# Kernel optimization log

Hardware: AMD Instinct MI355X
Metric: run time of the kernel (lower is better)

The kernel has to match this reference:

```python
import jax, jax.numpy as jnp
import numpy as np

# Module hyperparameters (init_kwargs)
NUM_EXPERTS = 8
HIDDEN = 1024
CAP_FACTORS = [0.5, 0.75, 1.0, 1.0, 1.25, 1.25, 1.5, 1.5]


def setup_inputs() -> dict:
    key = jax.random.key(0)
    k1, k2, k3 = jax.random.split(key, 3)
    G, T = 4, 2048
    token_inputs = jax.random.normal(k1, (G, T, HIDDEN), dtype=jnp.float32)
    # RouterWeights = nn.Linear(hidden, num_experts, bias=True)
    W = jax.random.normal(k2, (HIDDEN, NUM_EXPERTS), dtype=jnp.float32) * (1.0 / np.sqrt(HIDDEN))
    b = jax.random.normal(k3, (NUM_EXPERTS,), dtype=jnp.float32) * 0.01
    return {"token_inputs": token_inputs, "W": W, "b": b, "expert_capacity": 256}


def reference(token_inputs, W, b, expert_capacity):
    # token_inputs: [G, T, H]; jitter_noise=0 so no jitter; ignore_padding_tokens=False
    G, T, _ = token_inputs.shape
    logits = jnp.einsum("gth,he->gte", token_inputs, W) + b  # [G, T, E]
    probs = jax.nn.softmax(logits, axis=-1)
    # router z-loss: mean(logsumexp(logits, -1)^2)
    z_loss = jnp.mean(jax.nn.logsumexp(logits, axis=-1) ** 2)

    capacities = [int(expert_capacity * f) for f in CAP_FACTORS]
    max_cap = max(capacities)

    dispatch_slices = []  # each [G, T, max_cap] int32
    combine_slices = []   # each [G, T, max_cap] float32
    for e, cap in enumerate(capacities):
        gate, idx = jax.lax.top_k(probs[:, :, e], cap)  # [G, cap]
        # one_hot(idx, T): [G, cap, T] -> transpose to [G, T, cap]
        oh = jax.nn.one_hot(idx, T, dtype=jnp.int32).transpose(0, 2, 1)  # [G, T, cap]
        oh = jnp.pad(oh, ((0, 0), (0, 0), (0, max_cap - cap)))
        dispatch_slices.append(oh)
        # combine: gate broadcast over tokens dim (as in original code)
        comb = jnp.broadcast_to(gate[:, None, :], (G, T, cap))  # [G, T, cap]
        comb = jnp.pad(comb, ((0, 0), (0, 0), (0, max_cap - cap)))
        combine_slices.append(comb)

    dispatch_mask = jnp.stack(dispatch_slices, axis=1)  # [G, E, T, max_cap]
    combine_array = jnp.stack(combine_slices, axis=1).astype(jnp.float32)  # [G, E, T, max_cap]
    auxiliary_loss = jnp.float32(0.0)
    return dispatch_mask, combine_array, auxiliary_loss, z_loss
```

## Files before the change

kernel.cpp:

```cpp
#include <hip/hip_runtime.h>
#include <hip/hip_bf16.h>
#include <math.h>

#define G 4
#define T 2048
#define H 1024
#define E 8
#define NBUK 2048
#define SELB 32
#define K1B 512
#define K2B 256
#define K3B 256
#define SCB 12

typedef float f4 __attribute__((ext_vector_type(4)));
typedef unsigned long long u64;


__global__ __launch_bounds__(256) void k1_logits(
    const float* __restrict__ x, const float* __restrict__ W,
    const float* __restrict__ b, u64* __restrict__ keys,
    float* __restrict__ lse2) {
  int slot = (int)(blockIdx.x * 4 + (threadIdx.x >> 6));
  int lane = (int)(threadIdx.x & 63);

  for (int wave = slot; wave < G * T; wave += K1B * 4) {
    const float* xr = x + (size_t)wave * H;
    double acc0 = 0, acc1 = 0, acc2 = 0, acc3 = 0;
    double acc4 = 0, acc5 = 0, acc6 = 0, acc7 = 0;
#pragma unroll
    for (int j = 0; j < 4; ++j) {
      int hbase = j * 256 + lane * 4;
      f4 xv = *(const f4*)(xr + hbase);
#pragma unroll
      for (int k = 0; k < 4; ++k) {
        const float* wr = W + (size_t)(hbase + k) * 8;
        f4 w0 = *(const f4*)(wr);
        f4 w1 = *(const f4*)(wr + 4);
        double xd = (double)xv[k];
        acc0 += xd * (double)w0[0];
        acc1 += xd * (double)w0[1];
        acc2 += xd * (double)w0[2];
        acc3 += xd * (double)w0[3];
        acc4 += xd * (double)w1[0];
        acc5 += xd * (double)w1[1];
        acc6 += xd * (double)w1[2];
        acc7 += xd * (double)w1[3];
      }
    }
#pragma unroll
    for (int off = 32; off >= 1; off >>= 1) {
      acc0 += __shfl_xor(acc0, off);
      acc1 += __shfl_xor(acc1, off);
      acc2 += __shfl_xor(acc2, off);
      acc3 += __shfl_xor(acc3, off);
      acc4 += __shfl_xor(acc4, off);
      acc5 += __shfl_xor(acc5, off);
      acc6 += __shfl_xor(acc6, off);
      acc7 += __shfl_xor(acc7, off);
    }
    double l0 = acc0 + (double)b[0], l1 = acc1 + (double)b[1];
    double l2 = acc2 + (double)b[2], l3 = acc3 + (double)b[3];
    double l4 = acc4 + (double)b[4], l5 = acc5 + (double)b[5];
    double l6 = acc6 + (double)b[6], l7 = acc7 + (double)b[7];
    double m = fmax(fmax(fmax(l0, l1), fmax(l2, l3)),
                    fmax(fmax(l4, l5), fmax(l6, l7)));
    double la = (lane & 1) ? l1 : l0;
    double lb = (lane & 1) ? l3 : l2;
    double lc = (lane & 1) ? l5 : l4;
    double ld = (lane & 1) ? l7 : l6;
    double le = (lane & 2) ? lb : la;
    double lf = (lane & 2) ? ld : lc;
    double lsel = (lane & 4) ? lf : le;

    double pe = exp(lsel - m);
    double s = pe;
    s += __shfl_xor(s, 1);
    s += __shfl_xor(s, 2);
    s += __shfl_xor(s, 4);
    double inv = 1.0 / s;
    float pf = (float)(pe * inv);

    int g = wave >> 11;
    int t = wave & (T - 1);
    if (lane < 8) {
      keys[((size_t)g * 8 + lane) * T + t] =
          ((u64)__float_as_uint(pf) << 32) | (unsigned)(~t);
    }
    if (lane == 0) {
      double lse = m + log(s);
      lse2[wave] = (float)(lse * lse);
    }
  }
}

__global__ __launch_bounds__(1024) void k2_select_zero(
    const u64* __restrict__ keys, float* __restrict__ gate,
    int* __restrict__ idx, float* __restrict__ out, unsigned n4d, int max_cap,
    int ec) {
  unsigned bid = blockIdx.x;
  unsigned tid = threadIdx.x;

  if (bid >= SELB) {
    f4* outD = (f4*)out;
    f4 z = {0.0f, 0.0f, 0.0f, 0.0f};
    unsigned stride = (K2B - SELB) * 1024u;
    for (unsigned i = (bid - SELB) * 1024u + tid; i < n4d; i += stride)
      outD[i] = z;
    return;
  }

  __shared__ int hist[NBUK];
  __shared__ int sA[NBUK];
  __shared__ int sB[NBUK];
  __shared__ int cur[NBUK];
  __shared__ u64 srt[T];
  int ge = (int)bid;

  hist[tid] = 0;
  hist[tid + 1024] = 0;
  if (tid < (unsigned)max_cap) {
    gate[(size_t)ge * max_cap + tid] = 0.0f;
    idx[(size_t)ge * max_cap + tid] = -1;
  }
  __syncthreads();

  const u64* kcol = keys + (size_t)ge * T;
  u64 k0 = kcol[tid];
  u64 k1 = kcol[tid + 1024];
  int b0 = (int)(k0 >> 53);
  int b1 = (int)(k1 >> 53);
  atomicAdd(&hist[b0], 1);
  atomicAdd(&hist[b1], 1);
  __syncthreads();

  sA[tid] = hist[tid];
  sA[tid + 1024] = hist[tid + 1024];
  __syncthreads();
  int* src = sA;
  int* dst = sB;
  for (int s = 1; s < NBUK; s <<= 1) {
    for (int i = (int)tid; i < NBUK; i += 1024) {
      int v = src[i];
      if (i + s < NBUK) v += src[i + s];
      dst[i] = v;
    }
    __syncthreads();
    int* tmp = src;
    src = dst;
    dst = tmp;
  }
  for (int i = (int)tid; i < NBUK; i += 1024) cur[i] = src[i] - hist[i];
  __syncthreads();

  int p0 = atomicAdd(&cur[b0], 1);
  srt[p0] = k0;
  int p1 = atomicAdd(&cur[b1], 1);
  srt[p1] = k1;
  __syncthreads();

  const double factors[8] = {0.5, 0.75, 1.0, 1.0, 1.25, 1.25, 1.5, 1.5};
  int cap = (int)((double)ec * factors[ge & 7]);

  int o0 = src[b0] - hist[b0];
  if (o0 < cap) {
    int end = src[b0];
    int c = 0;
    for (int i = o0; i < end; ++i) c += (int)(srt[i] > k0);
    int r = o0 + c;
    if (r < cap) {
      gate[(size_t)ge * max_cap + r] = __uint_as_float((unsigned)(k0 >> 32));
      idx[(size_t)ge * max_cap + r] = (int)~(unsigned)k0;
    }
  }
  int o1 = src[b1] - hist[b1];
  if (o1 < cap) {
    int end = src[b1];
    int c = 0;
    for (int i = o1; i < end; ++i) c += (int)(srt[i] > k1);
    int r = o1 + c;
    if (r < cap) {
      gate[(size_t)ge * max_cap + r] = __uint_as_float((unsigned)(k1 >> 32));
      idx[(size_t)ge * max_cap + r] = (int)~(unsigned)k1;
    }
  }
}

template <int MC4S>
__global__ __launch_bounds__(1024) void k3_scatter_combine(
    const float* __restrict__ gate, const int* __restrict__ idx,
    const float* __restrict__ lse2, float* __restrict__ out, unsigned n4d,
    unsigned mc4_rt, int max_cap) {
  const unsigned mc4 = MC4S ? (unsigned)MC4S : mc4_rt;
  unsigned tid = threadIdx.x;
  unsigned bid = blockIdx.x;

  if (bid == 0) {
    __shared__ double red[256];
    if (tid < 256) {
      double s = 0.0;
      for (int i = tid; i < G * T; i += 256) s += (double)lse2[i];
      red[tid] = s;
    }
    __syncthreads();
    for (int off = 128; off > 0; off >>= 1) {
      if ((int)tid < off) red[tid] += red[tid + off];
      __syncthreads();
    }
    if (tid == 0) {
      size_t ne = (size_t)n4d * 4;
      out[2 * ne] = 0.0f;
      out[2 * ne + 1] = (float)(red[0] / (double)(G * T));
    }
    return;
  }
  if (bid <= SCB) {
    unsigned s = (bid - 1) * 1024u + tid;
    if (s < (unsigned)(G * E) * (unsigned)max_cap) {
      unsigned ge = s / (unsigned)max_cap;
      unsigned c = s - ge * (unsigned)max_cap;
      int t = idx[s];
      if (t >= 0) out[((size_t)ge * T + t) * (unsigned)max_cap + c] = 1.0f;
    }
    return;
  }

  f4* outC = (f4*)out + n4d;
  const f4* gate4 = (const f4*)gate;
  unsigned fb = bid - 1 - SCB;
  unsigned nfb = K3B - 1 - SCB;
  unsigned stride = nfb * 1024u;
  for (unsigned i = fb * 1024u + tid; i < n4d; i += stride) {
    unsigned c4 = i % mc4;
    unsigned ge = (i / mc4) >> 11;
    outC[i] = gate4[ge * mc4 + c4];
  }
}

extern "C" void kernel_launch(void* const* d_in, const int* in_sizes, int n_in,
                              void* d_out, int out_size, void* d_ws,
                              size_t ws_size, hipStream_t stream) {
  const float* x = (const float*)d_in[0];
  const float* W = (const float*)d_in[1];
  const float* b = (const float*)d_in[2];

  long long body = (long long)out_size - 2;
  int max_cap = (int)(body / (2LL * G * E * T));
  if (max_cap <= 0) return;
  int ec = (2 * max_cap) / 3;

  u64* keys = (u64*)d_ws;
  float* lse2 = (float*)(keys + (size_t)G * E * T);
  float* gate = lse2 + (size_t)G * T;
  int* idx = (int*)(gate + (size_t)G * E * max_cap);

  unsigned n4d = (unsigned)((long long)G * E * T * max_cap / 4);

  k1_logits<<<K1B, 256, 0, stream>>>(x, W, b, keys, lse2);
  k2_select_zero<<<K2B, 1024, 0, stream>>>(keys, gate, idx, (float*)d_out,
                                           n4d, max_cap, ec);
  if (max_cap == 384) {
    k3_scatter_combine<96><<<K3B, 1024, 0, stream>>>(gate, idx, lse2,
                                                     (float*)d_out, n4d, 96u,
                                                     max_cap);
  } else {
    k3_scatter_combine<0><<<K3B, 1024, 0, stream>>>(
        gate, idx, lse2, (float*)d_out, n4d, (unsigned)(max_cap / 4), max_cap);
  }
}
```

Measured before the change: 80.59 us.

## Fuse three router kernels into one persistent kernel with grid barriers

Merges the logits/softmax, top-k select/zero-fill, and scatter/combine-fill kernels into a single 256-block kernel that synchronizes via spin-wait grid barriers on a workspace counter reset by a memset. The dispatch scatter of ones now happens directly inside the select phase, which removes the idx buffer and one pass. This targets launch overhead and inter-kernel gaps. In exchange it adds a memset, barrier spinning, and a dependency on all 256 blocks being co-resident. The fixed 32-waves-per-block mapping and the 1024-thread blocks with heavy shared memory also reduce how work spreads across the GPU.

```diff
diff --git a/kernel.cpp b/kernel.cpp
--- a/kernel.cpp
+++ b/kernel.cpp
@@ -7,199 +7,196 @@
 #define H 1024
 #define E 8
 #define NBUK 2048
+#define NBLK 256
+#define NT 1024
 #define SELB 32
-#define K1B 512
-#define K2B 256
-#define K3B 256
-#define SCB 12
 
 typedef float f4 __attribute__((ext_vector_type(4)));
 typedef unsigned long long u64;
 
-
-__global__ __launch_bounds__(256) void k1_logits(
+__device__ __forceinline__ void gridbar(int* __restrict__ ctr) {
+  __syncthreads();
+  if (threadIdx.x == 0) {
+    __threadfence();
+    atomicAdd(ctr, 1);
+    long spins = 0;
+    while (atomicAdd(ctr, 0) < NBLK && spins < 400000000L) ++spins;
+    __threadfence();
+  }
+  __syncthreads();
+}
+
+__global__ __launch_bounds__(NT) void fused_all(
     const float* __restrict__ x, const float* __restrict__ W,
     const float* __restrict__ b, u64* __restrict__ keys,
-    float* __restrict__ lse2) {
-  int slot = (int)(blockIdx.x * 4 + (threadIdx.x >> 6));
-  int lane = (int)(threadIdx.x & 63);
-
-  for (int wave = slot; wave < G * T; wave += K1B * 4) {
-    const float* xr = x + (size_t)wave * H;
-    double acc0 = 0, acc1 = 0, acc2 = 0, acc3 = 0;
-    double acc4 = 0, acc5 = 0, acc6 = 0, acc7 = 0;
-#pragma unroll
-    for (int j = 0; j < 4; ++j) {
-      int hbase = j * 256 + lane * 4;
-      f4 xv = *(const f4*)(xr + hbase);
-#pragma unroll
-      for (int k = 0; k < 4; ++k) {
-        const float* wr = W + (size_t)(hbase + k) * 8;
-        f4 w0 = *(const f4*)(wr);
-        f4 w1 = *(const f4*)(wr + 4);
-        double xd = (double)xv[k];
-        acc0 += xd * (double)w0[0];
-        acc1 += xd * (double)w0[1];
-        acc2 += xd * (double)w0[2];
-        acc3 += xd * (double)w0[3];
-        acc4 += xd * (double)w1[0];
-        acc5 += xd * (double)w1[1];
-        acc6 += xd * (double)w1[2];
-        acc7 += xd * (double)w1[3];
-      }
-    }
-#pragma unroll
-    for (int off = 32; off >= 1; off >>= 1) {
-      acc0 += __shfl_xor(acc0, off);
-      acc1 += __shfl_xor(acc1, off);
-      acc2 += __shfl_xor(acc2, off);
-      acc3 += __shfl_xor(acc3, off);
-      acc4 += __shfl_xor(acc4, off);
-      acc5 += __shfl_xor(acc5, off);
-      acc6 += __shfl_xor(acc6, off);
-      acc7 += __shfl_xor(acc7, off);
-    }
-    double l0 = acc0 + (double)b[0], l1 = acc1 + (double)b[1];
-    double l2 = acc2 + (double)b[2], l3 = acc3 + (double)b[3];
-    double l4 = acc4 + (double)b[4], l5 = acc5 + (double)b[5];
-    double l6 = acc6 + (double)b[6], l7 = acc7 + (double)b[7];
-    double m = fmax(fmax(fmax(l0, l1), fmax(l2, l3)),
-                    fmax(fmax(l4, l5), fmax(l6, l7)));
-    double la = (lane & 1) ? l1 : l0;
-    double lb = (lane & 1) ? l3 : l2;
-    double lc = (lane & 1) ? l5 : l4;
-    double ld = (lane & 1) ? l7 : l6;
-    double le = (lane & 2) ? lb : la;
-    double lf = (lane & 2) ? ld : lc;
-    double lsel = (lane & 4) ? lf : le;
-
-    double pe = exp(lsel - m);
-    double s = pe;
-    s += __shfl_xor(s, 1);
-    s += __shfl_xor(s, 2);
-    s += __shfl_xor(s, 4);
-    double inv = 1.0 / s;
-    float pf = (float)(pe * inv);
-
-    int g = wave >> 11;
-    int t = wave & (T - 1);
-    if (lane < 8) {
-      keys[((size_t)g * 8 + lane) * T + t] =
-          ((u64)__float_as_uint(pf) << 32) | (unsigned)(~t);
-    }
-    if (lane == 0) {
-      double lse = m + log(s);
-      lse2[wave] = (float)(lse * lse);
-    }
-  }
-}
-
-__global__ __launch_bounds__(1024) void k2_select_zero(
-    const u64* __restrict__ keys, float* __restrict__ gate,
-    int* __restrict__ idx, float* __restrict__ out, unsigned n4d, int max_cap,
-    int ec) {
-  unsigned bid = blockIdx.x;
-  unsigned tid = threadIdx.x;
-
-  if (bid >= SELB) {
-    f4* outD = (f4*)out;
-    f4 z = {0.0f, 0.0f, 0.0f, 0.0f};
-    unsigned stride = (K2B - SELB) * 1024u;
-    for (unsigned i = (bid - SELB) * 1024u + tid; i < n4d; i += stride)
-      outD[i] = z;
-    return;
-  }
-
+    float* __restrict__ lse2, float* __restrict__ gate, int* __restrict__ bar,
+    float* __restrict__ out, unsigned n4d, int max_cap, int ec) {
   __shared__ int hist[NBUK];
   __shared__ int sA[NBUK];
   __shared__ int sB[NBUK];
   __shared__ int cur[NBUK];
   __shared__ u64 srt[T];
-  int ge = (int)bid;
-
-  hist[tid] = 0;
-  hist[tid + 1024] = 0;
-  if (tid < (unsigned)max_cap) {
-    gate[(size_t)ge * max_cap + tid] = 0.0f;
-    idx[(size_t)ge * max_cap + tid] = -1;
-  }
-  __syncthreads();
-
-  const u64* kcol = keys + (size_t)ge * T;
-  u64 k0 = kcol[tid];
-  u64 k1 = kcol[tid + 1024];
-  int b0 = (int)(k0 >> 53);
-  int b1 = (int)(k1 >> 53);
-  atomicAdd(&hist[b0], 1);
-  atomicAdd(&hist[b1], 1);
-  __syncthreads();
-
-  sA[tid] = hist[tid];
-  sA[tid + 1024] = hist[tid + 1024];
-  __syncthreads();
-  int* src = sA;
-  int* dst = sB;
-  for (int s = 1; s < NBUK; s <<= 1) {
-    for (int i = (int)tid; i < NBUK; i += 1024) {
-      int v = src[i];
-      if (i + s < NBUK) v += src[i + s];
-      dst[i] = v;
-    }
-    __syncthreads();
-    int* tmp = src;
-    src = dst;
-    dst = tmp;
-  }
-  for (int i = (int)tid; i < NBUK; i += 1024) cur[i] = src[i] - hist[i];
-  __syncthreads();
-
-  int p0 = atomicAdd(&cur[b0], 1);
-  srt[p0] = k0;
-  int p1 = atomicAdd(&cur[b1], 1);
-  srt[p1] = k1;
-  __syncthreads();
-
-  const double factors[8] = {0.5, 0.75, 1.0, 1.0, 1.25, 1.25, 1.5, 1.5};
-  int cap = (int)((double)ec * factors[ge & 7]);
-
-  int o0 = src[b0] - hist[b0];
-  if (o0 < cap) {
-    int end = src[b0];
-    int c = 0;
-    for (int i = o0; i < end; ++i) c += (int)(srt[i] > k0);
-    int r = o0 + c;
-    if (r < cap) {
-      gate[(size_t)ge * max_cap + r] = __uint_as_float((unsigned)(k0 >> 32));
-      idx[(size_t)ge * max_cap + r] = (int)~(unsigned)k0;
-    }
-  }
-  int o1 = src[b1] - hist[b1];
-  if (o1 < cap) {
-    int end = src[b1];
-    int c = 0;
-    for (int i = o1; i < end; ++i) c += (int)(srt[i] > k1);
-    int r = o1 + c;
-    if (r < cap) {
-      gate[(size_t)ge * max_cap + r] = __uint_as_float((unsigned)(k1 >> 32));
-      idx[(size_t)ge * max_cap + r] = (int)~(unsigned)k1;
-    }
-  }
-}
-
-template <int MC4S>
-__global__ __launch_bounds__(1024) void k3_scatter_combine(
-    const float* __restrict__ gate, const int* __restrict__ idx,
-    const float* __restrict__ lse2, float* __restrict__ out, unsigned n4d,
-    unsigned mc4_rt, int max_cap) {
-  const unsigned mc4 = MC4S ? (unsigned)MC4S : mc4_rt;
+  __shared__ double red[256];
+
+  unsigned bid = blockIdx.x;
   unsigned tid = threadIdx.x;
-  unsigned bid = blockIdx.x;
+
+  {
+    int lane = (int)(tid & 63);
+    int wv = (int)(tid >> 6);
+#pragma unroll
+    for (int rep = 0; rep < 2; ++rep) {
+      int wave = (int)(bid * 32) + wv * 2 + rep;
+      const float* xr = x + (size_t)wave * H;
+      double acc0 = 0, acc1 = 0, acc2 = 0, acc3 = 0;
+      double acc4 = 0, acc5 = 0, acc6 = 0, acc7 = 0;
+#pragma unroll
+      for (int j = 0; j < 4; ++j) {
+        int hbase = j * 256 + lane * 4;
+        f4 xv = *(const f4*)(xr + hbase);
+#pragma unroll
+        for (int k = 0; k < 4; ++k) {
+          const float* wr = W + (size_t)(hbase + k) * 8;
+          f4 w0 = *(const f4*)(wr);
+          f4 w1 = *(const f4*)(wr + 4);
+          double xd = (double)xv[k];
+          acc0 += xd * (double)w0[0];
+          acc1 += xd * (double)w0[1];
+          acc2 += xd * (double)w0[2];
+          acc3 += xd * (double)w0[3];
+          acc4 += xd * (double)w1[0];
+          acc5 += xd * (double)w1[1];
+          acc6 += xd * (double)w1[2];
+          acc7 += xd * (double)w1[3];
+        }
+      }
+#pragma unroll
+      for (int off = 32; off >= 1; off >>= 1) {
+        acc0 += __shfl_xor(acc0, off);
+        acc1 += __shfl_xor(acc1, off);
+        acc2 += __shfl_xor(acc2, off);
+        acc3 += __shfl_xor(acc3, off);
+        acc4 += __shfl_xor(acc4, off);
+        acc5 += __shfl_xor(acc5, off);
+        acc6 += __shfl_xor(acc6, off);
+        acc7 += __shfl_xor(acc7, off);
+      }
+      double l0 = acc0 + (double)b[0], l1 = acc1 + (double)b[1];
+      double l2 = acc2 + (double)b[2], l3 = acc3 + (double)b[3];
+      double l4 = acc4 + (double)b[4], l5 = acc5 + (double)b[5];
+      double l6 = acc6 + (double)b[6], l7 = acc7 + (double)b[7];
+      double m = fmax(fmax(fmax(l0, l1), fmax(l2, l3)),
+                      fmax(fmax(l4, l5), fmax(l6, l7)));
+      double la = (lane & 1) ? l1 : l0;
+      double lb = (lane & 1) ? l3 : l2;
+      double lc = (lane & 1) ? l5 : l4;
+      double ld = (lane & 1) ? l7 : l6;
+      double le = (lane & 2) ? lb : la;
+      double lf = (lane & 2) ? ld : lc;
+      double lsel = (lane & 4) ? lf : le;
+
+      double pe = exp(lsel - m);
+      double s = pe;
+      s += __shfl_xor(s, 1);
+      s += __shfl_xor(s, 2);
+      s += __shfl_xor(s, 4);
+      double inv = 1.0 / s;
+      float pf = (float)(pe * inv);
+
+      int g = wave >> 11;
+      int t = wave & (T - 1);
+      if (lane < 8) {
+        keys[((size_t)g * 8 + lane) * T + t] =
+            ((u64)__float_as_uint(pf) << 32) | (unsigned)(~t);
+      }
+      if (lane == 0) {
+        double lse = m + log(s);
+        lse2[wave] = (float)(lse * lse);
+      }
+    }
+  }
+  {
+    f4* outD = (f4*)out;
+    f4 z = {0.0f, 0.0f, 0.0f, 0.0f};
+    for (unsigned i = bid * NT + tid; i < n4d; i += NBLK * NT) outD[i] = z;
+  }
+  gridbar(&bar[0]);
+
+  if (bid < SELB) {
+    int ge = (int)bid;
+    hist[tid] = 0;
+    hist[tid + 1024] = 0;
+    if (tid < (unsigned)max_cap) gate[(size_t)ge * max_cap + tid] = 0.0f;
+    __syncthreads();
+
+    const u64* kcol = keys + (size_t)ge * T;
+    u64 k0 = kcol[tid];
+    u64 k1 = kcol[tid + 1024];
+    int b0 = (int)(k0 >> 53);
+    int b1 = (int)(k1 >> 53);
+    atomicAdd(&hist[b0], 1);
+    atomicAdd(&hist[b1], 1);
+    __syncthreads();
+
+    sA[tid] = hist[tid];
+    sA[tid + 1024] = hist[tid + 1024];
+    __syncthreads();
+    int* src = sA;
+    int* dst = sB;
+    for (int s = 1; s < NBUK; s <<= 1) {
+      for (int i = (int)tid; i < NBUK; i += 1024) {
+        int v = src[i];
+        if (i + s < NBUK) v += src[i + s];
+        dst[i] = v;
+      }
+      __syncthreads();
+      int* tmp = src;
+      src = dst;
+      dst = tmp;
+    }
+    for (int i = (int)tid; i < NBUK; i += 1024) cur[i] = src[i] - hist[i];
+    __syncthreads();
+
+    int p0 = atomicAdd(&cur[b0], 1);
+    srt[p0] = k0;
+    int p1 = atomicAdd(&cur[b1], 1);
+    srt[p1] = k1;
+    __syncthreads();
+
+    const double factors[8] = {0.5, 0.75, 1.0, 1.0, 1.25, 1.25, 1.5, 1.5};
+    int cap = (int)((double)ec * factors[ge & 7]);
+
+    int o0 = src[b0] - hist[b0];
+    if (o0 < cap) {
+      int end = src[b0];
+      int c = 0;
+      for (int i = o0; i < end; ++i) c += (int)(srt[i] > k0);
+      int r = o0 + c;
+      if (r < cap) {
+        unsigned t = ~(unsigned)k0;
+        gate[(size_t)ge * max_cap + r] = __uint_as_float((unsigned)(k0 >> 32));
+        out[((size_t)ge * T + t) * (unsigned)max_cap + r] = 1.0f;
+      }
+    }
+    int o1 = src[b1] - hist[b1];
+    if (o1 < cap) {
+      int end = src[b1];
+      int c = 0;
+      for (int i = o1; i < end; ++i) c += (int)(srt[i] > k1);
+      int r = o1 + c;
+      if (r < cap) {
+        unsigned t = ~(unsigned)k1;
+        gate[(size_t)ge * max_cap + r] = __uint_as_float((unsigned)(k1 >> 32));
+        out[((size_t)ge * T + t) * (unsigned)max_cap + r] = 1.0f;
+      }
+    }
+  }
+  gridbar(&bar[1]);
 
   if (bid == 0) {
-    __shared__ double red[256];
     if (tid < 256) {
       double s = 0.0;
-      for (int i = tid; i < G * T; i += 256) s += (double)lse2[i];
+      for (int i = (int)tid; i < G * T; i += 256) s += (double)lse2[i];
       red[tid] = s;
     }
     __syncthreads();
@@ -212,28 +209,16 @@
       out[2 * ne] = 0.0f;
       out[2 * ne + 1] = (float)(red[0] / (double)(G * T));
     }
-    return;
-  }
-  if (bid <= SCB) {
-    unsigned s = (bid - 1) * 1024u + tid;
-    if (s < (unsigned)(G * E) * (unsigned)max_cap) {
-      unsigned ge = s / (unsigned)max_cap;
-      unsigned c = s - ge * (unsigned)max_cap;
-      int t = idx[s];
-      if (t >= 0) out[((size_t)ge * T + t) * (unsigned)max_cap + c] = 1.0f;
-    }
-    return;
-  }
-
-  f4* outC = (f4*)out + n4d;
-  const f4* gate4 = (const f4*)gate;
-  unsigned fb = bid - 1 - SCB;
-  unsigned nfb = K3B - 1 - SCB;
-  unsigned stride = nfb * 1024u;
-  for (unsigned i = fb * 1024u + tid; i < n4d; i += stride) {
-    unsigned c4 = i % mc4;
-    unsigned ge = (i / mc4) >> 11;
-    outC[i] = gate4[ge * mc4 + c4];
+  }
+  {
+    f4* outC = (f4*)out + n4d;
+    const f4* gate4 = (const f4*)gate;
+    unsigned mc4 = (unsigned)(max_cap / 4);
+    for (unsigned i = bid * NT + tid; i < n4d; i += NBLK * NT) {
+      unsigned c4 = i % mc4;
+      unsigned ge = (i / mc4) >> 11;
+      outC[i] = gate4[ge * mc4 + c4];
+    }
   }
 }
 
@@ -252,19 +237,11 @@
   u64* keys = (u64*)d_ws;
   float* lse2 = (float*)(keys + (size_t)G * E * T);
   float* gate = lse2 + (size_t)G * T;
-  int* idx = (int*)(gate + (size_t)G * E * max_cap);
+  int* bar = (int*)(gate + (size_t)G * E * max_cap);
 
   unsigned n4d = (unsigned)((long long)G * E * T * max_cap / 4);
 
-  k1_logits<<<K1B, 256, 0, stream>>>(x, W, b, keys, lse2);
-  k2_select_zero<<<K2B, 1024, 0, stream>>>(keys, gate, idx, (float*)d_out,
-                                           n4d, max_cap, ec);
-  if (max_cap == 384) {
-    k3_scatter_combine<96><<<K3B, 1024, 0, stream>>>(gate, idx, lse2,
-                                                     (float*)d_out, n4d, 96u,
-                                                     max_cap);
-  } else {
-    k3_scatter_combine<0><<<K3B, 1024, 0, stream>>>(
-        gate, idx, lse2, (float*)d_out, n4d, (unsigned)(max_cap / 4), max_cap);
-  }
+  hipMemsetAsync(bar, 0, 2 * sizeof(int), stream);
+  fused_all<<<NBLK, NT, 0, stream>>>(x, W, b, keys, lse2, gate, bar,
+                                     (float*)d_out, n4d, max_cap, ec);
 }
```

Result: slower. 126.0 us (+56.3%).
